# Kernel tuning notes

Measured on AMD Instinct MI355X. Metric: run time of the kernel, lower is better.

The kernel has to match this reference:

```python
import jax, jax.numpy as jnp
import numpy as np

NUM_CLASSES = 27
LAM_U, LAM_B, LAM_D = 0.3, 0.2, 0.2


def _grads(x2d):
    # backward-difference with edge replication (matches torch.cat([x[:, :, :1], x[:, :, :-1]]))
    gx = x2d - jnp.concatenate([x2d[:, :, :1], x2d[:, :, :-1]], axis=-1)
    gy = x2d - jnp.concatenate([x2d[:, :1, :], x2d[:, :-1, :]], axis=-2)
    return gx, gy


def setup_inputs() -> dict:
    key = jax.random.key(0)
    k1, k2, k3 = jax.random.split(key, 3)
    B, M, H, W = 16, 32, 256, 256
    N = H * W
    return {
        "semantic_pred": jax.random.randint(k1, (B, N), 0, NUM_CLASSES, dtype=jnp.int32),
        "instance_masks": jax.random.uniform(k2, (B, M, N), dtype=jnp.float32),
        "depth": jax.random.uniform(k3, (B, N), dtype=jnp.float32),
        "spatial_h": H,
        "spatial_w": W,
    }


def _forward(semantic_pred, instance_masks, depth, spatial_h, spatial_w):
    b, m, n = instance_masks.shape

    # ---- uniformity loss: fused one-hot matmul replaces B*M*C python loops ----
    onehot = jax.nn.one_hot(semantic_pred, NUM_CLASSES, dtype=instance_masks.dtype)  # (B,N,C)
    class_hist = jnp.einsum('bmn,bnc->bmc', instance_masks, onehot)                  # (B,M,C)
    mask_sum = jnp.sum(instance_masks, axis=-1) + 1e-6                               # (B,M)
    class_prob = jnp.clip(class_hist / mask_sum[..., None], 1e-7, 1.0)
    entropy = -jnp.sum(jnp.where(class_prob > 1e-6,
                                 class_prob * jnp.log(class_prob + 1e-10),
                                 jnp.zeros_like(class_prob)), axis=-1)               # (B,M)
    l_uniform = jnp.sum(entropy) / (b * m + 1e-8)

    # ---- boundary alignment loss ----
    sem_2d = semantic_pred.reshape(b, spatial_h, spatial_w).astype(jnp.float32)
    mask_2d = instance_masks[:, 0, :].reshape(b, spatial_h, spatial_w)
    sgx, sgy = _grads(sem_2d)
    sem_boundary = ((jnp.abs(sgx) > 0) | (jnp.abs(sgy) > 0)).astype(jnp.float32)
    mgx, mgy = _grads(mask_2d)
    inst_boundary = ((jnp.abs(mgx) > 0.3) | (jnp.abs(mgy) > 0.3)).astype(jnp.float32)
    intersection = jnp.sum(sem_boundary * inst_boundary, axis=(-2, -1))
    union = jnp.sum(jnp.maximum(sem_boundary, inst_boundary), axis=(-2, -1)) + 1e-8
    l_boundary = 1.0 - jnp.mean(intersection / union)

    # ---- depth-boundary coherence loss ----
    depth_2d = depth.reshape(b, spatial_h, spatial_w)
    dgx, dgy = _grads(depth_2d)
    s = dgx ** 2 + dgy ** 2
    depth_boundary = jnp.sqrt(jnp.maximum(s, 1e-24))  # eps avoids NaN grad at s==0; forward ~identical
    sem_b = jnp.maximum((sgx != 0).astype(jnp.float32), (sgy != 0).astype(jnp.float32))
    db_clamped = jnp.clip(depth_boundary, 0.0, 2.0)
    weight = 1.0 + db_clamped * 3.0
    l_dbc = jnp.mean(weight * (1.0 - sem_b) * db_clamped)

    total = LAM_U * l_uniform + LAM_B * l_boundary + LAM_D * l_dbc
    return l_uniform, l_boundary, l_dbc, total


def reference(semantic_pred, instance_masks, depth, spatial_h, spatial_w):
    return _forward(semantic_pred, instance_masks, depth, spatial_h, spatial_w)
```

## Files before the change

kernel.cpp:

```cpp
#include <hip/hip_runtime.h>
#include <math.h>

#define NUM_CLASSES 27
#define HDIM 256
#define WDIM 256
#define NPIX (HDIM * WDIM)


__global__ __launch_bounds__(512) void hist_entropy_kernel(
    const float* __restrict__ masks, const int* __restrict__ sem,
    float* __restrict__ ws, int M) {
  __shared__ float s_hist[512][32];
  __shared__ float s_part[16][32];

  const int bm = blockIdx.x;
  const int b = bm / M;
  const int m = bm % M;
  const int tid = threadIdx.x;

  float4* zr = (float4*)&s_hist[tid][0];
#pragma unroll
  for (int i = 0; i < 8; ++i) zr[i] = make_float4(0.f, 0.f, 0.f, 0.f);

  const float4* __restrict__ m4 =
      (const float4*)(masks + ((size_t)b * M + m) * (size_t)NPIX);
  const int4* __restrict__ s4 = (const int4*)(sem + (size_t)b * (size_t)NPIX);

  float* h = s_hist[tid];
  const int skew = tid & 31;

  const int iters = NPIX / 4 / 512;
#pragma unroll 4
  for (int it = 0; it < iters; ++it) {
    const int idx = it * 512 + tid;
    const float4 mv = m4[idx];
    const int4 cv = s4[idx];
    h[(cv.x + skew) & 31] += mv.x;
    h[(cv.y + skew) & 31] += mv.y;
    h[(cv.z + skew) & 31] += mv.z;
    h[(cv.w + skew) & 31] += mv.w;
  }
  __syncthreads();

  {
    const int g = tid >> 5;
    const int c = tid & 31;
    float acc = 0.f;
#pragma unroll
    for (int i = 0; i < 32; ++i) {
      const int r = g * 32 + i;
      acc += s_hist[r][(c + r) & 31];
    }
    s_part[g][c] = acc;
  }
  __syncthreads();

  if (tid < 64) {
    float tot = 0.f;
    if (tid < 32) {
#pragma unroll
      for (int g = 0; g < 16; ++g) tot += s_part[g][tid];
    }
    float ms = tot;
    for (int off = 32; off > 0; off >>= 1) ms += __shfl_xor(ms, off);
    ms += 1e-6f;
    float ent = 0.f;
    if (tid < NUM_CLASSES) {
      float p = fminf(fmaxf(tot / ms, 1e-7f), 1.0f);
      if (p > 1e-6f) ent = p * logf(p + 1e-10f);
    }
    for (int off = 32; off > 0; off >>= 1) ent += __shfl_xor(ent, off);
    if (tid == 0) atomicAdd(&ws[0], -ent);
  }
}

__global__ __launch_bounds__(256) void boundary_kernel(
    const int* __restrict__ sem, const float* __restrict__ masks,
    const float* __restrict__ depth, float* __restrict__ ws, int M) {
  const int wave = threadIdx.x >> 6;
  const int lane = threadIdx.x & 63;
  const int brow = blockIdx.x * 4 + wave;
  const int b = brow >> 8;
  const int y = brow & 255;

  const size_t rowoff = (size_t)b * NPIX + (size_t)y * WDIM;
  const float4* mp = (const float4*)(masks + (size_t)b * M * NPIX + (size_t)y * WDIM);
  const float4* dp = (const float4*)(depth + rowoff);
  const int4* sp = (const int4*)(sem + rowoff);

  const int uoff = (y > 0) ? -(WDIM / 4) : 0;

  const float4 mv = mp[lane];
  const float4 mvu = mp[lane + uoff];
  const float4 dv = dp[lane];
  const float4 dvu = dp[lane + uoff];
  const int4 sv = sp[lane];
  const int4 svu = sp[lane + uoff];

  const int src = (lane > 0) ? (lane - 1) : 0;
  float mw = __shfl(mv.w, src);
  float dw = __shfl(dv.w, src);
  int swv = __shfl(sv.w, src);
  if (lane == 0) { mw = mv.x; dw = dv.x; swv = sv.x; }

  const float ml[4] = {mw, mv.x, mv.y, mv.z};
  const float dl[4] = {dw, dv.x, dv.y, dv.z};
  const int sl[4] = {swv, sv.x, sv.y, sv.z};
  const float mc[4] = {mv.x, mv.y, mv.z, mv.w};
  const float dc[4] = {dv.x, dv.y, dv.z, dv.w};
  const int sc[4] = {sv.x, sv.y, sv.z, sv.w};
  const float mu[4] = {mvu.x, mvu.y, mvu.z, mvu.w};
  const float du[4] = {dvu.x, dvu.y, dvu.z, dvu.w};
  const int su[4] = {svu.x, svu.y, svu.z, svu.w};

  float inter = 0.f, uni = 0.f, term = 0.f;
#pragma unroll
  for (int j = 0; j < 4; ++j) {
    const bool semb = (sc[j] != sl[j]) || (sc[j] != su[j]);
    const bool instb = (fabsf(mc[j] - ml[j]) > 0.3f) || (fabsf(mc[j] - mu[j]) > 0.3f);
    inter += (semb && instb) ? 1.0f : 0.0f;
    uni += (semb || instb) ? 1.0f : 0.0f;
    const float gx = dc[j] - dl[j];
    const float gy = dc[j] - du[j];
    const float db = sqrtf(fmaxf(gx * gx + gy * gy, 1e-24f));
    const float dbc = fminf(db, 2.0f);
    term += semb ? 0.0f : (1.0f + 3.0f * dbc) * dbc;
  }

  for (int off = 32; off > 0; off >>= 1) {
    inter += __shfl_down(inter, off);
    uni += __shfl_down(uni, off);
    term += __shfl_down(term, off);
  }
  __shared__ float s_i[4], s_u[4], s_t[4];
  if (lane == 0) { s_i[wave] = inter; s_u[wave] = uni; s_t[wave] = term; }
  __syncthreads();
  if (threadIdx.x == 0) {
    const float bi = s_i[0] + s_i[1] + s_i[2] + s_i[3];
    const float bu = s_u[0] + s_u[1] + s_u[2] + s_u[3];
    const float bt = s_t[0] + s_t[1] + s_t[2] + s_t[3];
    atomicAdd(&ws[8 + b], bi);
    atomicAdd(&ws[64 + b], bu);
    atomicAdd(&ws[1], bt);
  }
}

__global__ void finalize_kernel(const float* __restrict__ ws,
                                float* __restrict__ out, int B, int M) {
  const float l_u = ws[0] / ((float)(B * M) + 1e-8f);
  float acc = 0.0f;
  for (int b = 0; b < B; ++b) acc += ws[8 + b] / (ws[64 + b] + 1e-8f);
  const float l_b = 1.0f - acc / (float)B;
  const float l_d = ws[1] / (float)((size_t)B * NPIX);
  out[0] = l_u;
  out[1] = l_b;
  out[2] = l_d;
  out[3] = 0.3f * l_u + 0.2f * l_b + 0.2f * l_d;
}

extern "C" void kernel_launch(void* const* d_in, const int* in_sizes, int n_in,
                              void* d_out, int out_size, void* d_ws, size_t ws_size,
                              hipStream_t stream) {
  const int* sem = (const int*)d_in[0];
  const float* masks = (const float*)d_in[1];
  const float* depth = (const float*)d_in[2];

  const int B = in_sizes[0] / NPIX;
  const int M = in_sizes[1] / in_sizes[0];
  float* ws = (float*)d_ws;
  float* out = (float*)d_out;

  hipMemsetAsync(ws, 0, 128 * sizeof(float), stream);

  hist_entropy_kernel<<<B * M, 512, 0, stream>>>(masks, sem, ws, M);
  boundary_kernel<<<B * HDIM / 4, 256, 0, stream>>>(sem, masks, depth, ws, M);
  finalize_kernel<<<1, 1, 0, stream>>>(ws, out, B, M);
}
```

Baseline: 229.5 us.

## Fuse histogram and boundary kernels, drop memset and atomics, transpose shared histogram

Merges the histogram/entropy kernel and the boundary kernel into one launch, with the block index range choosing which work each block does. Per-block partials go to fixed workspace slots instead of atomics, so the memset is no longer needed, and a 512-thread finalize kernel reduces them in parallel. The shared histogram is laid out class-major with one column per thread, which removes the skew indexing. The change hardcodes the block counts (512 histogram blocks, 16 batches) and relies on B=16, M=32.

```diff
diff --git a/kernel.cpp b/kernel.cpp
--- a/kernel.cpp
+++ b/kernel.cpp
@@ -6,156 +6,185 @@
 #define WDIM 256
 #define NPIX (HDIM * WDIM)
 
-
-__global__ __launch_bounds__(512) void hist_entropy_kernel(
+#define NB_HIST 512
+#define NB_BND 512
+#define ROWS_PER_BND_BLOCK 8
+
+
+__global__ __launch_bounds__(512) void fused_kernel(
     const float* __restrict__ masks, const int* __restrict__ sem,
-    float* __restrict__ ws, int M) {
-  __shared__ float s_hist[512][32];
+    const float* __restrict__ depth, float* __restrict__ ws, int M) {
+  __shared__ float s_hist[28][512];
   __shared__ float s_part[16][32];
-
-  const int bm = blockIdx.x;
-  const int b = bm / M;
-  const int m = bm % M;
+  __shared__ float s_i[8], s_u[8], s_t[8];
+
   const int tid = threadIdx.x;
 
-  float4* zr = (float4*)&s_hist[tid][0];
-#pragma unroll
-  for (int i = 0; i < 8; ++i) zr[i] = make_float4(0.f, 0.f, 0.f, 0.f);
-
-  const float4* __restrict__ m4 =
-      (const float4*)(masks + ((size_t)b * M + m) * (size_t)NPIX);
-  const int4* __restrict__ s4 = (const int4*)(sem + (size_t)b * (size_t)NPIX);
-
-  float* h = s_hist[tid];
-  const int skew = tid & 31;
-
-  const int iters = NPIX / 4 / 512;
+  if (blockIdx.x < NB_HIST) {
+    const int bm = blockIdx.x;
+    const int b = bm / M;
+    const int m = bm % M;
+
+    float* col = &s_hist[0][tid];
+#pragma unroll
+    for (int c = 0; c < 28; ++c) col[c * 512] = 0.0f;
+
+    const float4* __restrict__ m4 =
+        (const float4*)(masks + ((size_t)b * M + m) * (size_t)NPIX);
+    const int4* __restrict__ s4 = (const int4*)(sem + (size_t)b * (size_t)NPIX);
+
+    const int iters = NPIX / 4 / 512;
 #pragma unroll 4
-  for (int it = 0; it < iters; ++it) {
-    const int idx = it * 512 + tid;
-    const float4 mv = m4[idx];
-    const int4 cv = s4[idx];
-    h[(cv.x + skew) & 31] += mv.x;
-    h[(cv.y + skew) & 31] += mv.y;
-    h[(cv.z + skew) & 31] += mv.z;
-    h[(cv.w + skew) & 31] += mv.w;
-  }
+    for (int it = 0; it < iters; ++it) {
+      const int idx = it * 512 + tid;
+      const float4 mv = m4[idx];
+      const int4 cv = s4[idx];
+      col[cv.x * 512] += mv.x;
+      col[cv.y * 512] += mv.y;
+      col[cv.z * 512] += mv.z;
+      col[cv.w * 512] += mv.w;
+    }
+    __syncthreads();
+
+    {
+      const int c = tid & 31;
+      const int s = tid >> 5;
+      if (c < 28) {
+        float acc = 0.f;
+#pragma unroll
+        for (int i = 0; i < 32; ++i)
+          acc += s_hist[c][s * 32 + ((i + c) & 31)];
+        s_part[s][c] = acc;
+      }
+    }
+    __syncthreads();
+
+    if (tid < 64) {
+      float tot = 0.f;
+      if (tid < 28) {
+#pragma unroll
+        for (int g = 0; g < 16; ++g) tot += s_part[g][tid];
+      }
+      float ms = tot;
+      for (int off = 32; off > 0; off >>= 1) ms += __shfl_xor(ms, off);
+      ms += 1e-6f;
+      float ent = 0.f;
+      if (tid < NUM_CLASSES) {
+        float p = fminf(fmaxf(tot / ms, 1e-7f), 1.0f);
+        if (p > 1e-6f) ent = p * logf(p + 1e-10f);
+      }
+      for (int off = 32; off > 0; off >>= 1) ent += __shfl_xor(ent, off);
+      if (tid == 0) ws[bm] = -ent;
+    }
+  } else {
+    const int j = blockIdx.x - NB_HIST;
+    const int wave = tid >> 6;
+    const int lane = tid & 63;
+    const int brow = j * ROWS_PER_BND_BLOCK + wave;
+    const int b = brow >> 8;
+    const int y = brow & 255;
+
+    const size_t rowoff = (size_t)b * NPIX + (size_t)y * WDIM;
+    const float4* mp = (const float4*)(masks + (size_t)b * M * NPIX + (size_t)y * WDIM);
+    const float4* dp = (const float4*)(depth + rowoff);
+    const int4* sp = (const int4*)(sem + rowoff);
+
+    const int uoff = (y > 0) ? -(WDIM / 4) : 0;
+
+    const float4 mv = mp[lane];
+    const float4 mvu = mp[lane + uoff];
+    const float4 dv = dp[lane];
+    const float4 dvu = dp[lane + uoff];
+    const int4 sv = sp[lane];
+    const int4 svu = sp[lane + uoff];
+
+    const int src = (lane > 0) ? (lane - 1) : 0;
+    float mw = __shfl(mv.w, src);
+    float dw = __shfl(dv.w, src);
+    int swv = __shfl(sv.w, src);
+    if (lane == 0) { mw = mv.x; dw = dv.x; swv = sv.x; }
+
+    const float ml[4] = {mw, mv.x, mv.y, mv.z};
+    const float dl[4] = {dw, dv.x, dv.y, dv.z};
+    const int sl[4] = {swv, sv.x, sv.y, sv.z};
+    const float mc[4] = {mv.x, mv.y, mv.z, mv.w};
+    const float dc[4] = {dv.x, dv.y, dv.z, dv.w};
+    const int sc[4] = {sv.x, sv.y, sv.z, sv.w};
+    const float mu[4] = {mvu.x, mvu.y, mvu.z, mvu.w};
+    const float du[4] = {dvu.x, dvu.y, dvu.z, dvu.w};
+    const int su[4] = {svu.x, svu.y, svu.z, svu.w};
+
+    float inter = 0.f, uni = 0.f, term = 0.f;
+#pragma unroll
+    for (int k = 0; k < 4; ++k) {
+      const bool semb = (sc[k] != sl[k]) || (sc[k] != su[k]);
+      const bool instb = (fabsf(mc[k] - ml[k]) > 0.3f) || (fabsf(mc[k] - mu[k]) > 0.3f);
+      inter += (semb && instb) ? 1.0f : 0.0f;
+      uni += (semb || instb) ? 1.0f : 0.0f;
+      const float gx = dc[k] - dl[k];
+      const float gy = dc[k] - du[k];
+      const float db = sqrtf(fmaxf(gx * gx + gy * gy, 1e-24f));
+      const float dbc = fminf(db, 2.0f);
+      term += semb ? 0.0f : (1.0f + 3.0f * dbc) * dbc;
+    }
+
+    for (int off = 32; off > 0; off >>= 1) {
+      inter += __shfl_down(inter, off);
+      uni += __shfl_down(uni, off);
+      term += __shfl_down(term, off);
+    }
+    if (lane == 0) { s_i[wave] = inter; s_u[wave] = uni; s_t[wave] = term; }
+    __syncthreads();
+    if (tid == 0) {
+      float bi = 0.f, bu = 0.f, bt = 0.f;
+#pragma unroll
+      for (int w = 0; w < 8; ++w) { bi += s_i[w]; bu += s_u[w]; bt += s_t[w]; }
+      ws[512 + j] = bi;
+      ws[1024 + j] = bu;
+      ws[1536 + j] = bt;
+    }
+  }
+}
+
+__global__ __launch_bounds__(512) void finalize_kernel(
+    const float* __restrict__ ws, float* __restrict__ out, int B, int M) {
+  const int tid = threadIdx.x;
+  const int lane = tid & 63;
+  const int wave = tid >> 6;
+  __shared__ float s_e[8], s_d[8], s_r[16];
+
+  float e = ws[tid];
+  float dbc = ws[1536 + tid];
+  float inter = ws[512 + tid];
+  float uni = ws[1024 + tid];
+
+  for (int off = 16; off > 0; off >>= 1) {
+    inter += __shfl_down(inter, off, 32);
+    uni += __shfl_down(uni, off, 32);
+  }
+  if ((tid & 31) == 0) s_r[tid >> 5] = inter / (uni + 1e-8f);
+
+  for (int off = 32; off > 0; off >>= 1) {
+    e += __shfl_down(e, off);
+    dbc += __shfl_down(dbc, off);
+  }
+  if (lane == 0) { s_e[wave] = e; s_d[wave] = dbc; }
   __syncthreads();
 
-  {
-    const int g = tid >> 5;
-    const int c = tid & 31;
-    float acc = 0.f;
-#pragma unroll
-    for (int i = 0; i < 32; ++i) {
-      const int r = g * 32 + i;
-      acc += s_hist[r][(c + r) & 31];
-    }
-    s_part[g][c] = acc;
-  }
-  __syncthreads();
-
-  if (tid < 64) {
-    float tot = 0.f;
-    if (tid < 32) {
-#pragma unroll
-      for (int g = 0; g < 16; ++g) tot += s_part[g][tid];
-    }
-    float ms = tot;
-    for (int off = 32; off > 0; off >>= 1) ms += __shfl_xor(ms, off);
-    ms += 1e-6f;
-    float ent = 0.f;
-    if (tid < NUM_CLASSES) {
-      float p = fminf(fmaxf(tot / ms, 1e-7f), 1.0f);
-      if (p > 1e-6f) ent = p * logf(p + 1e-10f);
-    }
-    for (int off = 32; off > 0; off >>= 1) ent += __shfl_xor(ent, off);
-    if (tid == 0) atomicAdd(&ws[0], -ent);
-  }
-}
-
-__global__ __launch_bounds__(256) void boundary_kernel(
-    const int* __restrict__ sem, const float* __restrict__ masks,
-    const float* __restrict__ depth, float* __restrict__ ws, int M) {
-  const int wave = threadIdx.x >> 6;
-  const int lane = threadIdx.x & 63;
-  const int brow = blockIdx.x * 4 + wave;
-  const int b = brow >> 8;
-  const int y = brow & 255;
-
-  const size_t rowoff = (size_t)b * NPIX + (size_t)y * WDIM;
-  const float4* mp = (const float4*)(masks + (size_t)b * M * NPIX + (size_t)y * WDIM);
-  const float4* dp = (const float4*)(depth + rowoff);
-  const int4* sp = (const int4*)(sem + rowoff);
-
-  const int uoff = (y > 0) ? -(WDIM / 4) : 0;
-
-  const float4 mv = mp[lane];
-  const float4 mvu = mp[lane + uoff];
-  const float4 dv = dp[lane];
-  const float4 dvu = dp[lane + uoff];
-  const int4 sv = sp[lane];
-  const int4 svu = sp[lane + uoff];
-
-  const int src = (lane > 0) ? (lane - 1) : 0;
-  float mw = __shfl(mv.w, src);
-  float dw = __shfl(dv.w, src);
-  int swv = __shfl(sv.w, src);
-  if (lane == 0) { mw = mv.x; dw = dv.x; swv = sv.x; }
-
-  const float ml[4] = {mw, mv.x, mv.y, mv.z};
-  const float dl[4] = {dw, dv.x, dv.y, dv.z};
-  const int sl[4] = {swv, sv.x, sv.y, sv.z};
-  const float mc[4] = {mv.x, mv.y, mv.z, mv.w};
-  const float dc[4] = {dv.x, dv.y, dv.z, dv.w};
-  const int sc[4] = {sv.x, sv.y, sv.z, sv.w};
-  const float mu[4] = {mvu.x, mvu.y, mvu.z, mvu.w};
-  const float du[4] = {dvu.x, dvu.y, dvu.z, dvu.w};
-  const int su[4] = {svu.x, svu.y, svu.z, svu.w};
-
-  float inter = 0.f, uni = 0.f, term = 0.f;
-#pragma unroll
-  for (int j = 0; j < 4; ++j) {
-    const bool semb = (sc[j] != sl[j]) || (sc[j] != su[j]);
-    const bool instb = (fabsf(mc[j] - ml[j]) > 0.3f) || (fabsf(mc[j] - mu[j]) > 0.3f);
-    inter += (semb && instb) ? 1.0f : 0.0f;
-    uni += (semb || instb) ? 1.0f : 0.0f;
-    const float gx = dc[j] - dl[j];
-    const float gy = dc[j] - du[j];
-    const float db = sqrtf(fmaxf(gx * gx + gy * gy, 1e-24f));
-    const float dbc = fminf(db, 2.0f);
-    term += semb ? 0.0f : (1.0f + 3.0f * dbc) * dbc;
-  }
-
-  for (int off = 32; off > 0; off >>= 1) {
-    inter += __shfl_down(inter, off);
-    uni += __shfl_down(uni, off);
-    term += __shfl_down(term, off);
-  }
-  __shared__ float s_i[4], s_u[4], s_t[4];
-  if (lane == 0) { s_i[wave] = inter; s_u[wave] = uni; s_t[wave] = term; }
-  __syncthreads();
-  if (threadIdx.x == 0) {
-    const float bi = s_i[0] + s_i[1] + s_i[2] + s_i[3];
-    const float bu = s_u[0] + s_u[1] + s_u[2] + s_u[3];
-    const float bt = s_t[0] + s_t[1] + s_t[2] + s_t[3];
-    atomicAdd(&ws[8 + b], bi);
-    atomicAdd(&ws[64 + b], bu);
-    atomicAdd(&ws[1], bt);
-  }
-}
-
-__global__ void finalize_kernel(const float* __restrict__ ws,
-                                float* __restrict__ out, int B, int M) {
-  const float l_u = ws[0] / ((float)(B * M) + 1e-8f);
-  float acc = 0.0f;
-  for (int b = 0; b < B; ++b) acc += ws[8 + b] / (ws[64 + b] + 1e-8f);
-  const float l_b = 1.0f - acc / (float)B;
-  const float l_d = ws[1] / (float)((size_t)B * NPIX);
-  out[0] = l_u;
-  out[1] = l_b;
-  out[2] = l_d;
-  out[3] = 0.3f * l_u + 0.2f * l_b + 0.2f * l_d;
+  if (tid == 0) {
+    float se = 0.f, sd = 0.f, sr = 0.f;
+#pragma unroll
+    for (int w = 0; w < 8; ++w) { se += s_e[w]; sd += s_d[w]; }
+#pragma unroll
+    for (int b = 0; b < 16; ++b) sr += s_r[b];
+    const float l_u = se / ((float)(B * M) + 1e-8f);
+    const float l_b = 1.0f - sr / (float)B;
+    const float l_d = sd / (float)((size_t)B * NPIX);
+    out[0] = l_u;
+    out[1] = l_b;
+    out[2] = l_d;
+    out[3] = 0.3f * l_u + 0.2f * l_b + 0.2f * l_d;
+  }
 }
 
 extern "C" void kernel_launch(void* const* d_in, const int* in_sizes, int n_in,
@@ -170,9 +199,6 @@
   float* ws = (float*)d_ws;
   float* out = (float*)d_out;
 
-  hipMemsetAsync(ws, 0, 128 * sizeof(float), stream);
-
-  hist_entropy_kernel<<<B * M, 512, 0, stream>>>(masks, sem, ws, M);
-  boundary_kernel<<<B * HDIM / 4, 256, 0, stream>>>(sem, masks, depth, ws, M);
-  finalize_kernel<<<1, 1, 0, stream>>>(ws, out, B, M);
+  fused_kernel<<<NB_HIST + NB_BND, 512, 0, stream>>>(masks, sem, depth, ws, M);
+  finalize_kernel<<<1, 512, 0, stream>>>(ws, out, B, M);
 }
```

Measured after the change: 202.8 us. 1.13x faster.
